# Kernel optimization log

Measured on AMD Instinct MI355X. Metric: run time of the kernel, lower is better.

The kernel has to match this reference:

```python
import jax, jax.numpy as jnp
import numpy as np

KSIZE = 11
SIGMA = 1.5
CHANNELS = 1


def _gaussian_kernel(size=KSIZE, sigma=SIGMA, channels=CHANNELS):
    coords = jnp.arange(size, dtype=jnp.float32) - size // 2
    g = jnp.exp(-coords ** 2 / (2.0 * sigma ** 2))
    g = g / g.sum()
    k2d = jnp.outer(g, g)  # [k, k]
    # depthwise kernel, OIHW with I=1 per group
    return jnp.broadcast_to(k2d, (channels, 1, size, size))


def _dwconv(x, k):
    pad = KSIZE // 2
    return jax.lax.conv_general_dilated(
        x, k, window_strides=(1, 1), padding=[(pad, pad), (pad, pad)],
        dimension_numbers=('NCHW', 'OIHW', 'NCHW'),
        feature_group_count=CHANNELS)


def setup_inputs() -> dict:
    key = jax.random.key(0)
    k1, k2 = jax.random.split(key)
    x_hat = jax.random.normal(k1, (64, 1, 512, 512), dtype=jnp.float32)
    x = jax.random.normal(k2, (64, 1, 512, 512), dtype=jnp.float32)
    kernel = _gaussian_kernel()
    return {"x_hat": x_hat, "x": x, "kernel": kernel}


def reference(x_hat, x, kernel):
    C1, C2 = 0.01 ** 2, 0.03 ** 2
    # shift [-1,1] -> [0,1]
    a = (x + 1.0) / 2.0          # 'x' in _ssim
    b = (x_hat + 1.0) / 2.0      # 'y' in _ssim
    mu_x = _dwconv(a, kernel)
    mu_y = _dwconv(b, kernel)
    mu_x2 = mu_x ** 2
    mu_y2 = mu_y ** 2
    mu_xy = mu_x * mu_y
    sig_x = _dwconv(a * a, kernel) - mu_x2
    sig_y = _dwconv(b * b, kernel) - mu_y2
    sig_xy = _dwconv(a * b, kernel) - mu_xy
    num = (2.0 * mu_xy + C1) * (2.0 * sig_xy + C2)
    den = (mu_x2 + mu_y2 + C1) * (sig_x + sig_y + C2)
    ssim = (num / (den + 1e-08)).mean()
    return 1.0 - ssim
```

## Files before the change

kernel.cpp:

```cpp
#include <hip/hip_runtime.h>

typedef float v2f __attribute__((ext_vector_type(2)));

#define IMG_W 512
#define IMG_H 512
#define RH    32
#define BW    128
#define NW    4
#define KS    11
#define KR    5
#define OFFP  9
#define LROWP (OFFP + BW + OFFP)
#define ROWS  (RH + 2 * KR)
#define NPH   44

struct Pf { float ax, ay, bx, by, lx, lb, rx, rb; };

__global__ __launch_bounds__(256, 2)
void ssim_main(const float* __restrict__ xhat,
               const float* __restrict__ x,
               const float* __restrict__ kern,
               float* __restrict__ accum)
{
    __shared__ __align__(16) float lds[NW][2][2 * LROWP];

    const int lane  = threadIdx.x & 63;
    const int wv    = threadIdx.x >> 6;
    const int strip = blockIdx.x & 15;
    const int img   = blockIdx.x >> 4;
    const int base  = wv * BW;
    const int R0    = strip * RH;
    const float* xp = x    + (size_t)img * (IMG_W * IMG_H);
    const float* hp = xhat + (size_t)img * (IMG_W * IMG_H);

    float g[KS];
    {
        const float inv = rsqrtf(kern[5 * KS + 5]);
        #pragma unroll
        for (int i = 0; i < KS; ++i) g[i] = kern[5 * KS + i] * inv;
    }

    const int  c0   = lane << 1;
    const bool lh   = lane < KR;
    const bool rhn  = lane >= 64 - KR;
    const int  lcol = base - KR + lane;
    const int  rcol = base + BW + (lane - (64 - KR));
    const int  lidx = OFFP - KR + lane;
    const int  ridx = OFFP + BW + (lane - (64 - KR));

    auto load_raw = [&](int rr) -> Pf {
        Pf p = {-1.f,-1.f,-1.f,-1.f,-1.f,-1.f,-1.f,-1.f};
        const int ri = R0 - KR + rr;
        if (ri >= 0 && ri < IMG_H) {
            const size_t ro = (size_t)ri * IMG_W;
            const float2 vx = *(const float2*)(xp + ro + base + c0);
            const float2 vh = *(const float2*)(hp + ro + base + c0);
            p.ax = vx.x;  p.ay = vx.y;
            p.bx = vh.x;  p.by = vh.y;
            if (lh && lcol >= 0) {
                p.lx = xp[ro + lcol];
                p.lb = hp[ro + lcol];
            }
            if (rhn && rcol < IMG_W) {
                p.rx = xp[ro + rcol];
                p.rb = hp[ro + rcol];
            }
        }
        return p;
    };

    v2f   h01r[KS][2];
    v2f   h23r[KS][2];
    float h4r [KS][2];
    float acc = 0.f;
    const float C1 = 1e-4f, C2 = 9e-4f;

    Pf pfA = load_raw(0);
    Pf pfB = load_raw(1);
    float* bufA = lds[wv][0];
    float* bufB = lds[wv][1];

    #pragma unroll 1
    for (int rblk = 0; rblk < NPH; rblk += KS) {
        #pragma unroll
        for (int p = 0; p < KS; ++p) {
            const int rr = rblk + p;
            if (rr < ROWS) {
                Pf&    cur = ((p & 1) == 0) ? pfA : pfB;
                float* buf = ((p & 1) == 0) ? bufA : bufB;

                *(float2*)&buf[2 * (OFFP + c0)] =
                    make_float2(fmaf(cur.ax, 0.5f, 0.5f), fmaf(cur.bx, 0.5f, 0.5f));
                *(float2*)&buf[2 * (OFFP + c0) + 2] =
                    make_float2(fmaf(cur.ay, 0.5f, 0.5f), fmaf(cur.by, 0.5f, 0.5f));
                if (lh)  *(float2*)&buf[2 * lidx] =
                    make_float2(fmaf(cur.lx, 0.5f, 0.5f), fmaf(cur.lb, 0.5f, 0.5f));
                if (rhn) *(float2*)&buf[2 * ridx] =
                    make_float2(fmaf(cur.rx, 0.5f, 0.5f), fmaf(cur.rb, 0.5f, 0.5f));

                const bool hasNext = (rr + 2 < ROWS);
                Pf nxt;
                if (hasNext) nxt = load_raw(rr + 2);

                __asm__ __volatile__("" ::: "memory");

                const float4* q = (const float4*)buf;
                float4 w[6];
                #pragma unroll
                for (int j = 0; j < 6; ++j) w[j] = q[lane + 2 + j];

                v2f h01[2] = {{0.f,0.f},{0.f,0.f}};
                v2f h23[2] = {{0.f,0.f},{0.f,0.f}};
                float h4[2] = {0.f, 0.f};
                #pragma unroll
                for (int t = 0; t < KS + 1; ++t) {
                    v2f ab;
                    ab.x = (t & 1) ? w[t >> 1].z : w[t >> 1].x;
                    ab.y = (t & 1) ? w[t >> 1].w : w[t >> 1].y;
                    const v2f  ab2 = ab * ab;
                    const float pab = ab.x * ab.y;
                    if (t < KS) {
                        const v2f wv2 = {g[t], g[t]};
                        h01[0] = __builtin_elementwise_fma(ab,  wv2, h01[0]);
                        h23[0] = __builtin_elementwise_fma(ab2, wv2, h23[0]);
                        h4[0]  = fmaf(pab, g[t], h4[0]);
                    }
                    if (t > 0) {
                        const v2f wv2 = {g[t - 1], g[t - 1]};
                        h01[1] = __builtin_elementwise_fma(ab,  wv2, h01[1]);
                        h23[1] = __builtin_elementwise_fma(ab2, wv2, h23[1]);
                        h4[1]  = fmaf(pab, g[t - 1], h4[1]);
                    }
                }
                #pragma unroll
                for (int c = 0; c < 2; ++c) {
                    h01r[p][c] = h01[c];
                    h23r[p][c] = h23[c];
                    h4r [p][c] = h4[c];
                }

                if (rr >= 2 * KR) {
                    v2f v01[2] = {{0.f,0.f},{0.f,0.f}};
                    v2f v23[2] = {{0.f,0.f},{0.f,0.f}};
                    float v4[2] = {0.f, 0.f};
                    #pragma unroll
                    for (int t = 0; t < KS; ++t) {
                        const int slot = (p + 1 + t) % KS;
                        const v2f wv2 = {g[t], g[t]};
                        #pragma unroll
                        for (int c = 0; c < 2; ++c) {
                            v01[c] = __builtin_elementwise_fma(h01r[slot][c], wv2, v01[c]);
                            v23[c] = __builtin_elementwise_fma(h23r[slot][c], wv2, v23[c]);
                            v4[c]  = fmaf(h4r[slot][c], g[t], v4[c]);
                        }
                    }
                    #pragma unroll
                    for (int c = 0; c < 2; ++c) {
                        const float mux  = v01[c].x, muy = v01[c].y;
                        const float mux2 = mux * mux;
                        const float muy2 = muy * muy;
                        const float muxy = mux * muy;
                        const float sx   = v23[c].x - mux2;
                        const float sy   = v23[c].y - muy2;
                        const float sxy  = v4[c]    - muxy;
                        const float num  = (2.f * muxy + C1) * (2.f * sxy + C2);
                        const float den  = (mux2 + muy2 + C1) * (sx + sy + C2);
                        acc = fmaf(num, __builtin_amdgcn_rcpf(den + 1e-8f), acc);
                    }
                }

                if (hasNext) cur = nxt;
            }
        }
        { Pf t = pfA; pfA = pfB; pfB = t; }
        { float* t = bufA; bufA = bufB; bufB = t; }
    }

    #pragma unroll
    for (int o = 32; o > 0; o >>= 1) acc += __shfl_down(acc, o, 64);
    if (lane == 0) atomicAdd(accum, acc);
}

__global__ void ssim_final(const float* __restrict__ accum,
                           float* __restrict__ out)
{
    out[0] = 1.0f - accum[0] * (1.0f / (64.0f * 512.0f * 512.0f));
}

extern "C" void kernel_launch(void* const* d_in, const int* in_sizes, int n_in,
                              void* d_out, int out_size, void* d_ws, size_t ws_size,
                              hipStream_t stream) {
    const float* xhat = (const float*)d_in[0];
    const float* xin  = (const float*)d_in[1];
    const float* kern = (const float*)d_in[2];
    float* out = (float*)d_out;
    float* ws  = (float*)d_ws;

    const int nimg = in_sizes[0] / (IMG_W * IMG_H);
    const int nblk = nimg * (IMG_H / RH);

    hipMemsetAsync(ws, 0, sizeof(float), stream);
    ssim_main<<<nblk, 64 * NW, 0, stream>>>(xhat, xin, kern, ws);
    ssim_final<<<1, 1, 0, stream>>>(ws, out);
}
```

Baseline: 235.1 us.

## Replace unrolled ring-buffer row loop with rolled loop and register shift window

Swaps the 11-way unrolled row loop (ring-buffer indexing, double-buffered LDS, two-rows-ahead prefetch) for a simple rolled loop. It uses a single LDS buffer per wave, prefetches only one row ahead, and shifts the horizontal-result registers down each row. The h4 accumulators are packed into a v2f so the vertical pass can use packed FMA. This shrinks code size and may simplify register allocation, but adds about 50 register moves per row and leaves less time to hide global load latency.

```diff
diff --git a/kernel.cpp b/kernel.cpp
--- a/kernel.cpp
+++ b/kernel.cpp
@@ -12,7 +12,6 @@
 #define OFFP  9
 #define LROWP (OFFP + BW + OFFP)
 #define ROWS  (RH + 2 * KR)
-#define NPH   44
 
 struct Pf { float ax, ay, bx, by, lx, lb, rx, rb; };
 
@@ -22,7 +21,7 @@
                const float* __restrict__ kern,
                float* __restrict__ accum)
 {
-    __shared__ __align__(16) float lds[NW][2][2 * LROWP];
+    __shared__ __align__(16) float lds[NW][2 * LROWP];
 
     const int lane  = threadIdx.x & 63;
     const int wv    = threadIdx.x >> 6;
@@ -48,6 +47,8 @@
     const int  lidx = OFFP - KR + lane;
     const int  ridx = OFFP + BW + (lane - (64 - KR));
 
+    float* buf = lds[wv];
+
     auto load_raw = [&](int rr) -> Pf {
         Pf p = {-1.f,-1.f,-1.f,-1.f,-1.f,-1.f,-1.f,-1.f};
         const int ri = R0 - KR + rr;
@@ -57,123 +58,103 @@
             const float2 vh = *(const float2*)(hp + ro + base + c0);
             p.ax = vx.x;  p.ay = vx.y;
             p.bx = vh.x;  p.by = vh.y;
-            if (lh && lcol >= 0) {
-                p.lx = xp[ro + lcol];
-                p.lb = hp[ro + lcol];
-            }
-            if (rhn && rcol < IMG_W) {
-                p.rx = xp[ro + rcol];
-                p.rb = hp[ro + rcol];
-            }
+            if (lh && lcol >= 0)    { p.lx = xp[ro + lcol]; p.lb = hp[ro + lcol]; }
+            if (rhn && rcol < IMG_W){ p.rx = xp[ro + rcol]; p.rb = hp[ro + rcol]; }
         }
         return p;
     };
 
-    v2f   h01r[KS][2];
-    v2f   h23r[KS][2];
-    float h4r [KS][2];
+    v2f h01r[KS][2];
+    v2f h23r[KS][2];
+    v2f h4r [KS];
     float acc = 0.f;
     const float C1 = 1e-4f, C2 = 9e-4f;
 
-    Pf pfA = load_raw(0);
-    Pf pfB = load_raw(1);
-    float* bufA = lds[wv][0];
-    float* bufB = lds[wv][1];
+    Pf cur = load_raw(0);
 
     #pragma unroll 1
-    for (int rblk = 0; rblk < NPH; rblk += KS) {
+    for (int rr = 0; rr < ROWS; ++rr) {
+        *(float2*)&buf[2 * (OFFP + c0)] =
+            make_float2(fmaf(cur.ax, 0.5f, 0.5f), fmaf(cur.bx, 0.5f, 0.5f));
+        *(float2*)&buf[2 * (OFFP + c0) + 2] =
+            make_float2(fmaf(cur.ay, 0.5f, 0.5f), fmaf(cur.by, 0.5f, 0.5f));
+        if (lh)  *(float2*)&buf[2 * lidx] =
+            make_float2(fmaf(cur.lx, 0.5f, 0.5f), fmaf(cur.lb, 0.5f, 0.5f));
+        if (rhn) *(float2*)&buf[2 * ridx] =
+            make_float2(fmaf(cur.rx, 0.5f, 0.5f), fmaf(cur.rb, 0.5f, 0.5f));
+
+        const Pf nxt = load_raw(rr + 1);
+
+        __asm__ __volatile__("" ::: "memory");
+
+        const float4* q = (const float4*)buf;
+        float4 w[6];
         #pragma unroll
-        for (int p = 0; p < KS; ++p) {
-            const int rr = rblk + p;
-            if (rr < ROWS) {
-                Pf&    cur = ((p & 1) == 0) ? pfA : pfB;
-                float* buf = ((p & 1) == 0) ? bufA : bufB;
+        for (int j = 0; j < 6; ++j) w[j] = q[lane + 2 + j];
 
-                *(float2*)&buf[2 * (OFFP + c0)] =
-                    make_float2(fmaf(cur.ax, 0.5f, 0.5f), fmaf(cur.bx, 0.5f, 0.5f));
-                *(float2*)&buf[2 * (OFFP + c0) + 2] =
-                    make_float2(fmaf(cur.ay, 0.5f, 0.5f), fmaf(cur.by, 0.5f, 0.5f));
-                if (lh)  *(float2*)&buf[2 * lidx] =
-                    make_float2(fmaf(cur.lx, 0.5f, 0.5f), fmaf(cur.lb, 0.5f, 0.5f));
-                if (rhn) *(float2*)&buf[2 * ridx] =
-                    make_float2(fmaf(cur.rx, 0.5f, 0.5f), fmaf(cur.rb, 0.5f, 0.5f));
-
-                const bool hasNext = (rr + 2 < ROWS);
-                Pf nxt;
-                if (hasNext) nxt = load_raw(rr + 2);
-
-                __asm__ __volatile__("" ::: "memory");
-
-                const float4* q = (const float4*)buf;
-                float4 w[6];
-                #pragma unroll
-                for (int j = 0; j < 6; ++j) w[j] = q[lane + 2 + j];
-
-                v2f h01[2] = {{0.f,0.f},{0.f,0.f}};
-                v2f h23[2] = {{0.f,0.f},{0.f,0.f}};
-                float h4[2] = {0.f, 0.f};
-                #pragma unroll
-                for (int t = 0; t < KS + 1; ++t) {
-                    v2f ab;
-                    ab.x = (t & 1) ? w[t >> 1].z : w[t >> 1].x;
-                    ab.y = (t & 1) ? w[t >> 1].w : w[t >> 1].y;
-                    const v2f  ab2 = ab * ab;
-                    const float pab = ab.x * ab.y;
-                    if (t < KS) {
-                        const v2f wv2 = {g[t], g[t]};
-                        h01[0] = __builtin_elementwise_fma(ab,  wv2, h01[0]);
-                        h23[0] = __builtin_elementwise_fma(ab2, wv2, h23[0]);
-                        h4[0]  = fmaf(pab, g[t], h4[0]);
-                    }
-                    if (t > 0) {
-                        const v2f wv2 = {g[t - 1], g[t - 1]};
-                        h01[1] = __builtin_elementwise_fma(ab,  wv2, h01[1]);
-                        h23[1] = __builtin_elementwise_fma(ab2, wv2, h23[1]);
-                        h4[1]  = fmaf(pab, g[t - 1], h4[1]);
-                    }
-                }
-                #pragma unroll
-                for (int c = 0; c < 2; ++c) {
-                    h01r[p][c] = h01[c];
-                    h23r[p][c] = h23[c];
-                    h4r [p][c] = h4[c];
-                }
-
-                if (rr >= 2 * KR) {
-                    v2f v01[2] = {{0.f,0.f},{0.f,0.f}};
-                    v2f v23[2] = {{0.f,0.f},{0.f,0.f}};
-                    float v4[2] = {0.f, 0.f};
-                    #pragma unroll
-                    for (int t = 0; t < KS; ++t) {
-                        const int slot = (p + 1 + t) % KS;
-                        const v2f wv2 = {g[t], g[t]};
-                        #pragma unroll
-                        for (int c = 0; c < 2; ++c) {
-                            v01[c] = __builtin_elementwise_fma(h01r[slot][c], wv2, v01[c]);
-                            v23[c] = __builtin_elementwise_fma(h23r[slot][c], wv2, v23[c]);
-                            v4[c]  = fmaf(h4r[slot][c], g[t], v4[c]);
-                        }
-                    }
-                    #pragma unroll
-                    for (int c = 0; c < 2; ++c) {
-                        const float mux  = v01[c].x, muy = v01[c].y;
-                        const float mux2 = mux * mux;
-                        const float muy2 = muy * muy;
-                        const float muxy = mux * muy;
-                        const float sx   = v23[c].x - mux2;
-                        const float sy   = v23[c].y - muy2;
-                        const float sxy  = v4[c]    - muxy;
-                        const float num  = (2.f * muxy + C1) * (2.f * sxy + C2);
-                        const float den  = (mux2 + muy2 + C1) * (sx + sy + C2);
-                        acc = fmaf(num, __builtin_amdgcn_rcpf(den + 1e-8f), acc);
-                    }
-                }
-
-                if (hasNext) cur = nxt;
+        v2f h01[2] = {{0.f,0.f},{0.f,0.f}};
+        v2f h23[2] = {{0.f,0.f},{0.f,0.f}};
+        v2f h4v    = {0.f, 0.f};
+        #pragma unroll
+        for (int t = 0; t < KS + 1; ++t) {
+            v2f ab;
+            ab.x = (t & 1) ? w[t >> 1].z : w[t >> 1].x;
+            ab.y = (t & 1) ? w[t >> 1].w : w[t >> 1].y;
+            const v2f  ab2 = ab * ab;
+            const float pab = ab.x * ab.y;
+            if (t < KS) {
+                const v2f wv2 = {g[t], g[t]};
+                h01[0] = __builtin_elementwise_fma(ab,  wv2, h01[0]);
+                h23[0] = __builtin_elementwise_fma(ab2, wv2, h23[0]);
+                h4v.x  = fmaf(pab, g[t], h4v.x);
+            }
+            if (t > 0) {
+                const v2f wv2 = {g[t - 1], g[t - 1]};
+                h01[1] = __builtin_elementwise_fma(ab,  wv2, h01[1]);
+                h23[1] = __builtin_elementwise_fma(ab2, wv2, h23[1]);
+                h4v.y  = fmaf(pab, g[t - 1], h4v.y);
             }
         }
-        { Pf t = pfA; pfA = pfB; pfB = t; }
-        { float* t = bufA; bufA = bufB; bufB = t; }
+
+        #pragma unroll
+        for (int s = 0; s < KS - 1; ++s) {
+            h01r[s][0] = h01r[s + 1][0];  h01r[s][1] = h01r[s + 1][1];
+            h23r[s][0] = h23r[s + 1][0];  h23r[s][1] = h23r[s + 1][1];
+            h4r [s]    = h4r [s + 1];
+        }
+        h01r[KS - 1][0] = h01[0];  h01r[KS - 1][1] = h01[1];
+        h23r[KS - 1][0] = h23[0];  h23r[KS - 1][1] = h23[1];
+        h4r [KS - 1]    = h4v;
+
+        if (rr >= 2 * KR) {
+            v2f v01[2] = {{0.f,0.f},{0.f,0.f}};
+            v2f v23[2] = {{0.f,0.f},{0.f,0.f}};
+            v2f v4     = {0.f, 0.f};
+            #pragma unroll
+            for (int t = 0; t < KS; ++t) {
+                const v2f wv2 = {g[t], g[t]};
+                v01[0] = __builtin_elementwise_fma(h01r[t][0], wv2, v01[0]);
+                v01[1] = __builtin_elementwise_fma(h01r[t][1], wv2, v01[1]);
+                v23[0] = __builtin_elementwise_fma(h23r[t][0], wv2, v23[0]);
+                v23[1] = __builtin_elementwise_fma(h23r[t][1], wv2, v23[1]);
+                v4     = __builtin_elementwise_fma(h4r[t],     wv2, v4);
+            }
+            #pragma unroll
+            for (int c = 0; c < 2; ++c) {
+                const float mux  = v01[c].x, muy = v01[c].y;
+                const float mux2 = mux * mux;
+                const float muy2 = muy * muy;
+                const float muxy = mux * muy;
+                const float sx   = v23[c].x - mux2;
+                const float sy   = v23[c].y - muy2;
+                const float sxy  = ((c == 0) ? v4.x : v4.y) - muxy;
+                const float num  = (2.f * muxy + C1) * (2.f * sxy + C2);
+                const float den  = (mux2 + muy2 + C1) * (sx + sy + C2);
+                acc = fmaf(num, __builtin_amdgcn_rcpf(den + 1e-8f), acc);
+            }
+        }
+
+        cur = nxt;
     }
 
     #pragma unroll
```

Measured after the change: 252.7 us. +7.5%, slower.
